# Optimization experiments

Hardware: AMD Instinct MI355X
Metric: run time of the kernel (lower is better)

## Reference

```python
import jax, jax.numpy as jnp
import numpy as np

N_NODES = 100_000
N_EDGES = 1_600_000
F_NODE = 4
F_EDGE = 5
H = 64
EDGE_DIM = 2 * H + F_EDGE  # 133


def setup_inputs() -> dict:
    key = jax.random.key(0)
    ks = jax.random.split(key, 24)
    s = 0.05
    inp = {
        "node_feat": jax.random.normal(ks[0], (N_NODES, F_NODE), jnp.float32),
        "edge_feat": jax.random.normal(ks[1], (N_EDGES, F_EDGE), jnp.float32),
        "src": jax.random.randint(ks[2], (N_EDGES,), 0, N_NODES, jnp.int32),
        "dst": jax.random.randint(ks[3], (N_EDGES,), 0, N_NODES, jnp.int32),
        # SAGEConv 1 (DGL mean aggregator: fc_self(h) + fc_neigh(mean_neigh(h)) + bias)
        "W1s": jax.random.normal(ks[4], (F_NODE, H), jnp.float32) * s,
        "W1n": jax.random.normal(ks[5], (F_NODE, H), jnp.float32) * s,
        "b1": jnp.zeros((H,), jnp.float32),
        # SAGEConv 2
        "W2s": jax.random.normal(ks[6], (H, H), jnp.float32) * s,
        "W2n": jax.random.normal(ks[7], (H, H), jnp.float32) * s,
        "b2": jnp.zeros((H,), jnp.float32),
        # nodeprocess: Linear(F_NODE? no -> applied to h which is H-dim) Linear(H? )
        # NOTE: original declares nn.Linear(num_node_features, hidden) but applies it to h (H-dim);
        # we follow the applied shape, Linear(H, H), so the math is runnable and consistent.
        "Wnp": jax.random.normal(ks[8], (H, H), jnp.float32) * s,
        "bnp": jnp.zeros((H,), jnp.float32),
        # edgeprocess: Linear(EDGE_DIM, H) -> tanh -> Linear(H, 1)
        "We1": jax.random.normal(ks[9], (EDGE_DIM, H), jnp.float32) * s,
        "be1": jnp.zeros((H,), jnp.float32),
        "We2": jax.random.normal(ks[10], (H, 1), jnp.float32) * s,
        "be2": jnp.zeros((1,), jnp.float32),
        # lin1: Linear(EDGE_DIM, H); lin2: Linear(H, 1)
        "Wl1": jax.random.normal(ks[11], (EDGE_DIM, H), jnp.float32) * s,
        "bl1": jnp.zeros((H,), jnp.float32),
        "Wl2": jax.random.normal(ks[12], (H, 1), jnp.float32) * s,
        "bl2": jnp.zeros((1,), jnp.float32),
    }
    return inp


def _sage_mean(h, src, dst, Ws, Wn, b, inv_deg):
    # project first (cheaper: N x d instead of E x d), then gather+scatter-mean
    msg = (h @ Wn)[src]                                    # [E, H]
    agg = jax.ops.segment_sum(msg, dst, num_segments=h.shape[0]) * inv_deg
    return h @ Ws + agg + b


def reference(node_feat, edge_feat, src, dst,
              W1s, W1n, b1, W2s, W2n, b2,
              Wnp, bnp, We1, be1, We2, be2,
              Wl1, bl1, Wl2, bl2):
    n = node_feat.shape[0]
    deg = jax.ops.segment_sum(jnp.ones_like(dst, jnp.float32), dst, num_segments=n)
    inv_deg = (1.0 / jnp.maximum(deg, 1.0))[:, None]       # [N,1]

    h = jax.nn.relu(_sage_mean(node_feat, src, dst, W1s, W1n, b1, inv_deg))
    h = jax.nn.relu(_sage_mean(h, src, dst, W2s, W2n, b2, inv_deg))

    h_src = jax.nn.relu(h[src] @ Wnp + bnp)                # [E, H]
    h_dst = jax.nn.relu(h[dst] @ Wnp + bnp)                # [E, H]
    ef = jnp.concatenate([h_src, h_dst, edge_feat], axis=1)  # [E, 133]

    w = jax.nn.sigmoid(jnp.tanh(ef @ We1 + be1) @ We2 + be2)  # [E, 1]
    efw = ef * w
    out = jax.nn.relu(efw @ Wl1 + bl1)                     # dropout: eval mode (identity)
    return out @ Wl2 + bl2                                 # [E, 1]
```

## Files before the change

### kernel.cpp

```cpp
#include <hip/hip_runtime.h>
#include <math.h>


__device__ __forceinline__ float fast_tanh(float x) {
    x = fminf(fmaxf(x, -15.f), 15.f);
    float e2 = __expf(2.f * x);
    return (e2 - 1.f) * __builtin_amdgcn_rcpf(e2 + 1.f);
}
__device__ __forceinline__ float fast_sigmoid(float x) {
    x = fminf(fmaxf(x, -60.f), 60.f);
    return __builtin_amdgcn_rcpf(1.f + __expf(-x));
}
__device__ __forceinline__ unsigned short f2bf(float f) {
    unsigned u = __float_as_uint(f);
    u = u + 0x7FFFu + ((u >> 16) & 1u);
    return (unsigned short)(u >> 16);
}
__device__ __forceinline__ unsigned pack2bf(float lo, float hi) {
    return ((unsigned)f2bf(hi) << 16) | (unsigned)f2bf(lo);
}
__device__ __forceinline__ float bflo(unsigned u) { return __uint_as_float(u << 16); }
__device__ __forceinline__ float bfhi(unsigned u) { return __uint_as_float(u & 0xFFFF0000u); }

__device__ __forceinline__ float dpp_sum16(float x) {
    int t;
    t = __builtin_amdgcn_update_dpp(0, __float_as_int(x), 0xB1, 0xF, 0xF, true);
    x += __int_as_float(t);
    t = __builtin_amdgcn_update_dpp(0, __float_as_int(x), 0x4E, 0xF, 0xF, true);
    x += __int_as_float(t);
    t = __builtin_amdgcn_update_dpp(0, __float_as_int(x), 0x141, 0xF, 0xF, true);
    x += __int_as_float(t);
    t = __builtin_amdgcn_update_dpp(0, __float_as_int(x), 0x140, 0xF, 0xF, true);
    x += __int_as_float(t);
    return x;
}

__global__ void rank_k(const int* __restrict__ dst, int* __restrict__ deg,
                       int* __restrict__ rank, int E) {
    int e = blockIdx.x * blockDim.x + threadIdx.x;
    if (e < E) rank[e] = atomicAdd(&deg[dst[e]], 1);
}

__global__ void scan1_k(const int* __restrict__ deg, int* __restrict__ off,
                        int* __restrict__ bsum, int N) {
    __shared__ int tmp[256];
    int i = blockIdx.x * 256 + threadIdx.x;
    int v = (i < N) ? deg[i] : 0;
    tmp[threadIdx.x] = v;
    __syncthreads();
#pragma unroll
    for (int s = 1; s < 256; s <<= 1) {
        int t = (threadIdx.x >= s) ? tmp[threadIdx.x - s] : 0;
        __syncthreads();
        tmp[threadIdx.x] += t;
        __syncthreads();
    }
    if (i < N) off[i] = tmp[threadIdx.x] - v;
    if (threadIdx.x == 255) bsum[blockIdx.x] = tmp[255];
}

__global__ void scan2_k(int* __restrict__ bsum, int nb) {
    __shared__ int tmp[512];
    int i = threadIdx.x;
    int v = (i < nb) ? bsum[i] : 0;
    tmp[i] = v;
    __syncthreads();
#pragma unroll
    for (int s = 1; s < 512; s <<= 1) {
        int t = (i >= s) ? tmp[i - s] : 0;
        __syncthreads();
        tmp[i] += t;
        __syncthreads();
    }
    if (i < nb) bsum[i] = tmp[i] - v;
}

__global__ void scan3_k(int* __restrict__ off, const int* __restrict__ bsum,
                        int N, int E) {
    int i = blockIdx.x * 256 + threadIdx.x;
    if (i < N) off[i] += bsum[blockIdx.x];
    if (i == 0) off[N] = E;
}

__global__ void fill2_k(const int* __restrict__ src, const int* __restrict__ dst,
                        const int* __restrict__ off, const int* __restrict__ rank,
                        int2* __restrict__ csr, int* __restrict__ dstp, int E) {
    int e = blockIdx.x * blockDim.x + threadIdx.x;
    if (e >= E) return;
    int d = dst[e];
    int pos = off[d] + rank[e];
    csr[pos] = make_int2(src[e], e);
    dstp[pos] = d;
}

__global__ __launch_bounds__(256, 8)
void aggh1f_k(const int* __restrict__ off, const int2* __restrict__ csr,
              const float* __restrict__ nf,
              const float* __restrict__ W1s, const float* __restrict__ W1n,
              const float* __restrict__ b1, unsigned* __restrict__ h1b, int N) {
    int n = blockIdx.x * 16 + (threadIdx.x >> 4);
    if (n >= N) return;
    int q = threadIdx.x & 15;
    int s0 = off[n], s1 = off[n + 1];
    const float4* nf4 = (const float4*)nf;
    float4 a = {0.f, 0.f, 0.f, 0.f};
    for (int i = s0 + q; i < s1; i += 16) {
        float4 r = nf4[(unsigned)csr[i].x];
        a.x += r.x; a.y += r.y; a.z += r.z; a.w += r.w;
    }
    a.x = dpp_sum16(a.x);
    a.y = dpp_sum16(a.y);
    a.z = dpp_sum16(a.z);
    a.w = dpp_sum16(a.w);
    float invd = 1.f / fmaxf((float)(s1 - s0), 1.f);
    a.x *= invd; a.y *= invd; a.z *= invd; a.w *= invd;
    float4 r = nf4[(unsigned)n];
    const int j0 = q << 2;
    float4 acc = *(const float4*)&b1[j0];
#pragma unroll
    for (int k = 0; k < 4; ++k) {
        float rk = (k == 0) ? r.x : (k == 1) ? r.y : (k == 2) ? r.z : r.w;
        float ak = (k == 0) ? a.x : (k == 1) ? a.y : (k == 2) ? a.z : a.w;
        float4 ws = *(const float4*)&W1s[k * 64 + j0];
        float4 wn = *(const float4*)&W1n[k * 64 + j0];
        acc.x = fmaf(rk, ws.x, acc.x); acc.y = fmaf(rk, ws.y, acc.y);
        acc.z = fmaf(rk, ws.z, acc.z); acc.w = fmaf(rk, ws.w, acc.w);
        acc.x = fmaf(ak, wn.x, acc.x); acc.y = fmaf(ak, wn.y, acc.y);
        acc.z = fmaf(ak, wn.z, acc.z); acc.w = fmaf(ak, wn.w, acc.w);
    }
    uint2 pk;
    pk.x = pack2bf(fmaxf(acc.x, 0.f), fmaxf(acc.y, 0.f));
    pk.y = pack2bf(fmaxf(acc.z, 0.f), fmaxf(acc.w, 0.f));
    *(uint2*)&h1b[(unsigned)n * 32u + (q << 1)] = pk;
}

__global__ __launch_bounds__(256, 8)
void gatherh1_k(const int* __restrict__ off, const int2* __restrict__ csr,
                const uint4* __restrict__ h1b4, uint4* __restrict__ ah1b4, int N) {
    int n = blockIdx.x * 4 + (threadIdx.x >> 6);
    if (n >= N) return;
    int l = threadIdx.x & 63;
    int g = l >> 3, q = l & 7;
    int s0 = off[n], s1 = off[n + 1];
    float a0 = 0.f, a1 = 0.f, a2 = 0.f, a3 = 0.f;
    float a4 = 0.f, a5 = 0.f, a6 = 0.f, a7 = 0.f;
    int i = s0;
    for (; i + 16 <= s1; i += 16) {
        int r0 = csr[i + g].x;
        int r1 = csr[i + 8 + g].x;
        uint4 v0 = h1b4[(unsigned)r0 * 8u + q];
        uint4 v1 = h1b4[(unsigned)r1 * 8u + q];
        a0 += bflo(v0.x) + bflo(v1.x); a1 += bfhi(v0.x) + bfhi(v1.x);
        a2 += bflo(v0.y) + bflo(v1.y); a3 += bfhi(v0.y) + bfhi(v1.y);
        a4 += bflo(v0.z) + bflo(v1.z); a5 += bfhi(v0.z) + bfhi(v1.z);
        a6 += bflo(v0.w) + bflo(v1.w); a7 += bfhi(v0.w) + bfhi(v1.w);
    }
    for (; i + 8 <= s1; i += 8) {
        int r = csr[i + g].x;
        uint4 v = h1b4[(unsigned)r * 8u + q];
        a0 += bflo(v.x); a1 += bfhi(v.x);
        a2 += bflo(v.y); a3 += bfhi(v.y);
        a4 += bflo(v.z); a5 += bfhi(v.z);
        a6 += bflo(v.w); a7 += bfhi(v.w);
    }
    int rem = s1 - i;
    if (g < rem) {
        int r = csr[i + g].x;
        uint4 v = h1b4[(unsigned)r * 8u + q];
        a0 += bflo(v.x); a1 += bfhi(v.x);
        a2 += bflo(v.y); a3 += bfhi(v.y);
        a4 += bflo(v.z); a5 += bfhi(v.z);
        a6 += bflo(v.w); a7 += bfhi(v.w);
    }
#pragma unroll
    for (int m = 8; m <= 32; m <<= 1) {
        a0 += __shfl_xor(a0, m); a1 += __shfl_xor(a1, m);
        a2 += __shfl_xor(a2, m); a3 += __shfl_xor(a3, m);
        a4 += __shfl_xor(a4, m); a5 += __shfl_xor(a5, m);
        a6 += __shfl_xor(a6, m); a7 += __shfl_xor(a7, m);
    }
    if (l < 8) {
        float invd = 1.f / fmaxf((float)(s1 - s0), 1.f);
        uint4 pk;
        pk.x = pack2bf(a0 * invd, a1 * invd);
        pk.y = pack2bf(a2 * invd, a3 * invd);
        pk.z = pack2bf(a4 * invd, a5 * invd);
        pk.w = pack2bf(a6 * invd, a7 * invd);
        ah1b4[(unsigned)n * 8u + q] = pk;
    }
}

__device__ __forceinline__ void mac64(const float (*hT)[68], const float (*wt)[64],
                                      int rr, int cr, float acc[4][4]) {
#pragma unroll 8
    for (int k = 0; k < 64; ++k) {
        float4 a = *(const float4*)&hT[k][rr];
        float4 w = *(const float4*)&wt[k][cr];
        acc[0][0] = fmaf(a.x, w.x, acc[0][0]); acc[0][1] = fmaf(a.x, w.y, acc[0][1]);
        acc[0][2] = fmaf(a.x, w.z, acc[0][2]); acc[0][3] = fmaf(a.x, w.w, acc[0][3]);
        acc[1][0] = fmaf(a.y, w.x, acc[1][0]); acc[1][1] = fmaf(a.y, w.y, acc[1][1]);
        acc[1][2] = fmaf(a.y, w.z, acc[1][2]); acc[1][3] = fmaf(a.y, w.w, acc[1][3]);
        acc[2][0] = fmaf(a.z, w.x, acc[2][0]); acc[2][1] = fmaf(a.z, w.y, acc[2][1]);
        acc[2][2] = fmaf(a.z, w.z, acc[2][2]); acc[2][3] = fmaf(a.z, w.w, acc[2][3]);
        acc[3][0] = fmaf(a.w, w.x, acc[3][0]); acc[3][1] = fmaf(a.w, w.y, acc[3][1]);
        acc[3][2] = fmaf(a.w, w.z, acc[3][2]); acc[3][3] = fmaf(a.w, w.w, acc[3][3]);
    }
}

__global__ __launch_bounds__(256, 4)
void node_mlp_k(const unsigned* __restrict__ h1b, const unsigned* __restrict__ ah1b,
                const float* __restrict__ W2s, const float* __restrict__ W2n,
                const float* __restrict__ b2, const float* __restrict__ Wnp,
                const float* __restrict__ bnp, const float* __restrict__ We1,
                const float* __restrict__ Wl1, const float* __restrict__ be1,
                unsigned short* __restrict__ ST, int N) {
    __shared__ __align__(16) float hT[64][68];
    __shared__ __align__(16) float wt[64][64];
    const int t = threadIdx.x;
    const int m0 = blockIdx.x * 64;
    const int cr = (t & 15) << 2, rr = (t >> 4) << 2;
    float acc[4][4] = {};

#pragma unroll
    for (int it = 0; it < 8; ++it) {
        int u = it * 256 + t;
        int m = u >> 5, p = u & 31;
        int row = m0 + m;
        unsigned v = (row < N) ? h1b[(unsigned)row * 32u + p] : 0u;
        hT[2 * p][m] = bflo(v);
        hT[2 * p + 1][m] = bfhi(v);
    }
#pragma unroll
    for (int it = 0; it < 16; ++it) {
        int k = it * 4 + (t >> 6), c = t & 63;
        wt[k][c] = W2s[k * 64 + c];
    }
    __syncthreads();
    mac64(hT, wt, rr, cr, acc);
    __syncthreads();

#pragma unroll
    for (int it = 0; it < 8; ++it) {
        int u = it * 256 + t;
        int m = u >> 5, p = u & 31;
        int row = m0 + m;
        unsigned v = (row < N) ? ah1b[(unsigned)row * 32u + p] : 0u;
        hT[2 * p][m] = bflo(v);
        hT[2 * p + 1][m] = bfhi(v);
    }
#pragma unroll
    for (int it = 0; it < 16; ++it) {
        int k = it * 4 + (t >> 6), c = t & 63;
        wt[k][c] = W2n[k * 64 + c];
    }
    __syncthreads();
    mac64(hT, wt, rr, cr, acc);
    __syncthreads();

#pragma unroll
    for (int i = 0; i < 4; ++i)
#pragma unroll
        for (int q = 0; q < 4; ++q)
            hT[cr + q][rr + i] = fmaxf(acc[i][q] + b2[cr + q], 0.f);
#pragma unroll
    for (int it = 0; it < 16; ++it) {
        int k = it * 4 + (t >> 6), c = t & 63;
        wt[k][c] = Wnp[k * 64 + c];
    }
    __syncthreads();
    float ac2[4][4] = {};
    mac64(hT, wt, rr, cr, ac2);
    __syncthreads();

#pragma unroll
    for (int i = 0; i < 4; ++i)
#pragma unroll
        for (int q = 0; q < 4; ++q)
            hT[cr + q][rr + i] = fmaxf(ac2[i][q] + bnp[cr + q], 0.f);
    __syncthreads();

    for (int cb = 0; cb < 4; ++cb) {
        if (cb) __syncthreads();
#pragma unroll
        for (int it = 0; it < 16; ++it) {
            int k = it * 4 + (t >> 6), c = t & 63;
            int cglob = cb * 64 + c;
            int half = cglob >> 7, cc = cglob & 127;
            int jj = cc >> 1, p = cc & 1;
            const float* W = p ? Wl1 : We1;
            wt[k][c] = W[(half * 64 + k) * 64 + jj];
        }
        __syncthreads();
        float ac3[4][4] = {};
        mac64(hT, wt, rr, cr, ac3);
        float bz0 = 0.f, bz2 = 0.f;
        if (cb >= 2) {
            int jj0 = ((cb * 64 + cr) & 127) >> 1;
            bz0 = be1[jj0];
            bz2 = be1[jj0 + 1];
        }
#pragma unroll
        for (int i = 0; i < 4; ++i) {
            int row = m0 + rr + i;
            if (row >= N) continue;
            ushort4 pk;
            pk.x = f2bf(ac3[i][0] + bz0); pk.y = f2bf(ac3[i][1]);
            pk.z = f2bf(ac3[i][2] + bz2); pk.w = f2bf(ac3[i][3]);
            *(ushort4*)&ST[(unsigned)row * 256u + cb * 64 + cr] = pk;
        }
    }
}

struct P8 {
    int2 seA, seB;
    int dnA, dnB;
    uint4 pwA, swA, pwB, swB;
    float eA0, eA1, eA2, eA3, eA4;
    float eB0, eB1, eB2, eB3, eB4;
    bool actA, actB;
};

__device__ __forceinline__ P8 pref_pair(int c, int nwaves, int nch, int E,
                                        int g, int j0,
                                        const int2* __restrict__ csr,
                                        const int* __restrict__ dstp,
                                        const float* __restrict__ ef,
                                        const unsigned* __restrict__ ST32) {
    P8 p;
    int sA = c * 4 + g;
    int cB = c + nwaves;
    int sB = cB * 4 + g;
    p.actA = (c < nch) && (sA < E);
    p.actB = (cB < nch) && (sB < E);
    unsigned uA = p.actA ? (unsigned)sA : 0u;
    unsigned uB = p.actB ? (unsigned)sB : 0u;
    p.dnA = dstp[uA];
    p.dnB = dstp[uB];
    p.seA = csr[uA];
    p.seB = csr[uB];
    p.pwA = *(const uint4*)&ST32[(unsigned)p.dnA * 128u + 64u + (unsigned)j0];
    p.pwB = *(const uint4*)&ST32[(unsigned)p.dnB * 128u + 64u + (unsigned)j0];
    p.swA = *(const uint4*)&ST32[(unsigned)p.seA.x * 128u + (unsigned)j0];
    p.swB = *(const uint4*)&ST32[(unsigned)p.seB.x * 128u + (unsigned)j0];
    const float* epA = ef + (unsigned)p.seA.y * 5u;
    const float* epB = ef + (unsigned)p.seB.y * 5u;
    p.eA0 = epA[0]; p.eA1 = epA[1]; p.eA2 = epA[2]; p.eA3 = epA[3]; p.eA4 = epA[4];
    p.eB0 = epB[0]; p.eB1 = epB[1]; p.eB2 = epB[2]; p.eB3 = epB[3]; p.eB4 = epB[4];
    return p;
}

__global__ void edge_k(const int2* __restrict__ csr, const int* __restrict__ dstp,
                       const float* __restrict__ ef, const unsigned* __restrict__ ST32,
                       const float* __restrict__ We1,
                       const float* __restrict__ We2, const float* __restrict__ be2,
                       const float* __restrict__ Wl1, const float* __restrict__ bl1,
                       const float* __restrict__ Wl2, const float* __restrict__ bl2,
                       float* __restrict__ out, int E, int nwaves) {
    const int l = threadIdx.x & 63;
    const int g = l >> 4;
    const int q = l & 15;
    const int j0 = q << 2;
    const int wid = blockIdx.x * (blockDim.x >> 6) + (threadIdx.x >> 6);

    float4 wet[5], wlt[5];
#pragma unroll
    for (int k = 0; k < 5; ++k) {
        wet[k] = *(const float4*)&We1[(128 + k) * 64 + j0];
        wlt[k] = *(const float4*)&Wl1[(128 + k) * 64 + j0];
    }
    const float4 vwe2 = *(const float4*)&We2[j0];
    const float4 vbl1 = *(const float4*)&bl1[j0];
    const float4 vwl2 = *(const float4*)&Wl2[j0];
    const float vbe2 = be2[0], vbl2 = bl2[0];

    const int nch = (E + 3) >> 2;
    const int step = 2 * nwaves;

#define KS(EK, K) \
    t4.x = fmaf(EK, wet[K].x, t4.x); t4.y = fmaf(EK, wet[K].y, t4.y); \
    t4.z = fmaf(EK, wet[K].z, t4.z); t4.w = fmaf(EK, wet[K].w, t4.w); \
    u4.x = fmaf(EK, wlt[K].x, u4.x); u4.y = fmaf(EK, wlt[K].y, u4.y); \
    u4.z = fmaf(EK, wlt[K].z, u4.z); u4.w = fmaf(EK, wlt[K].w, u4.w);

    P8 p = pref_pair(wid, nwaves, nch, E, g, j0, csr, dstp, ef, ST32);
    for (int c = wid; c < nch; ) {
        int cn = c + step;
        P8 pn = pref_pair(cn, nwaves, nch, E, g, j0, csr, dstp, ef, ST32);

        {
            float4 t4 = {bflo(p.swA.x) + bflo(p.pwA.x),
                         bflo(p.swA.y) + bflo(p.pwA.y),
                         bflo(p.swA.z) + bflo(p.pwA.z),
                         bflo(p.swA.w) + bflo(p.pwA.w)};
            float4 u4 = {bfhi(p.swA.x) + bfhi(p.pwA.x), bfhi(p.swA.y) + bfhi(p.pwA.y),
                         bfhi(p.swA.z) + bfhi(p.pwA.z), bfhi(p.swA.w) + bfhi(p.pwA.w)};
            KS(p.eA0, 0) KS(p.eA1, 1) KS(p.eA2, 2) KS(p.eA3, 3) KS(p.eA4, 4)
            float z = fast_tanh(t4.x) * vwe2.x + fast_tanh(t4.y) * vwe2.y
                    + fast_tanh(t4.z) * vwe2.z + fast_tanh(t4.w) * vwe2.w;
            z = dpp_sum16(z);
            float w = fast_sigmoid(z + vbe2);
            float o = fmaxf(fmaf(w, u4.x, vbl1.x), 0.f) * vwl2.x
                    + fmaxf(fmaf(w, u4.y, vbl1.y), 0.f) * vwl2.y
                    + fmaxf(fmaf(w, u4.z, vbl1.z), 0.f) * vwl2.z
                    + fmaxf(fmaf(w, u4.w, vbl1.w), 0.f) * vwl2.w;
            o = dpp_sum16(o);
            if (q == 0 && p.actA) out[(unsigned)p.seA.y] = o + vbl2;
        }
        {
            float4 t4 = {bflo(p.swB.x) + bflo(p.pwB.x),
                         bflo(p.swB.y) + bflo(p.pwB.y),
                         bflo(p.swB.z) + bflo(p.pwB.z),
                         bflo(p.swB.w) + bflo(p.pwB.w)};
            float4 u4 = {bfhi(p.swB.x) + bfhi(p.pwB.x), bfhi(p.swB.y) + bfhi(p.pwB.y),
                         bfhi(p.swB.z) + bfhi(p.pwB.z), bfhi(p.swB.w) + bfhi(p.pwB.w)};
            KS(p.eB0, 0) KS(p.eB1, 1) KS(p.eB2, 2) KS(p.eB3, 3) KS(p.eB4, 4)
            float z = fast_tanh(t4.x) * vwe2.x + fast_tanh(t4.y) * vwe2.y
                    + fast_tanh(t4.z) * vwe2.z + fast_tanh(t4.w) * vwe2.w;
            z = dpp_sum16(z);
            float w = fast_sigmoid(z + vbe2);
            float o = fmaxf(fmaf(w, u4.x, vbl1.x), 0.f) * vwl2.x
                    + fmaxf(fmaf(w, u4.y, vbl1.y), 0.f) * vwl2.y
                    + fmaxf(fmaf(w, u4.z, vbl1.z), 0.f) * vwl2.z
                    + fmaxf(fmaf(w, u4.w, vbl1.w), 0.f) * vwl2.w;
            o = dpp_sum16(o);
            if (q == 0 && p.actB) out[(unsigned)p.seB.y] = o + vbl2;
        }
        p = pn;
        c = cn;
    }
#undef KS
}

extern "C" void kernel_launch(void* const* d_in, const int* in_sizes, int n_in,
                              void* d_out, int out_size, void* d_ws, size_t ws_size,
                              hipStream_t stream) {
    const float* nf  = (const float*)d_in[0];
    const float* ef  = (const float*)d_in[1];
    const int*   src = (const int*)d_in[2];
    const int*   dst = (const int*)d_in[3];
    const float* W1s = (const float*)d_in[4];
    const float* W1n = (const float*)d_in[5];
    const float* b1  = (const float*)d_in[6];
    const float* W2s = (const float*)d_in[7];
    const float* W2n = (const float*)d_in[8];
    const float* b2  = (const float*)d_in[9];
    const float* Wnp = (const float*)d_in[10];
    const float* bnp = (const float*)d_in[11];
    const float* We1 = (const float*)d_in[12];
    const float* be1 = (const float*)d_in[13];
    const float* We2 = (const float*)d_in[14];
    const float* be2 = (const float*)d_in[15];
    const float* Wl1 = (const float*)d_in[16];
    const float* bl1 = (const float*)d_in[17];
    const float* Wl2 = (const float*)d_in[18];
    const float* bl2 = (const float*)d_in[19];

    const int N = in_sizes[0] / 4;
    const int E = in_sizes[2];

    float* wsf = (float*)d_ws;
    unsigned short* ST = (unsigned short*)wsf;
    unsigned* ah1b = (unsigned*)(wsf + (size_t)128 * N);
    int* dstp = (int*)(wsf + (size_t)160 * N);
    unsigned* h1b  = (unsigned*)(wsf + (size_t)192 * N);
    int2* csr  = (int2*)(wsf + (size_t)224 * N);
    int*  rank = (int*)(wsf + (size_t)256 * N);
    int*  deg  = (int*)(wsf + (size_t)272 * N);
    int*  off  = deg + N;
    int*  bsum = off + N + 1;
    float* out = (float*)d_out;

    const int nblkN1 = (N + 255) / 256;
    const int nblkE  = (E + 255) / 256;
    const int nblkNw4 = (N + 3) / 4;
    const int nblkN16 = (N + 15) / 16;
    const int gemmx  = (N + 63) / 64;
    const int EDGE_BLOCKS = 3072;
    const int nwaves = EDGE_BLOCKS * 4;

    hipMemsetAsync(deg, 0, (size_t)N * sizeof(int), stream);
    rank_k<<<nblkE, 256, 0, stream>>>(dst, deg, rank, E);
    scan1_k<<<nblkN1, 256, 0, stream>>>(deg, off, bsum, N);
    scan2_k<<<1, 512, 0, stream>>>(bsum, nblkN1);
    scan3_k<<<nblkN1, 256, 0, stream>>>(off, bsum, N, E);
    fill2_k<<<nblkE, 256, 0, stream>>>(src, dst, off, rank, csr, dstp, E);

    aggh1f_k<<<nblkN16, 256, 0, stream>>>(off, csr, nf, W1s, W1n, b1, h1b, N);

    gatherh1_k<<<nblkNw4, 256, 0, stream>>>(off, csr, (const uint4*)h1b,
                                            (uint4*)ah1b, N);

    node_mlp_k<<<gemmx, 256, 0, stream>>>(h1b, ah1b, W2s, W2n, b2,
                                          Wnp, bnp, We1, Wl1, be1, ST, N);

    edge_k<<<EDGE_BLOCKS, 256, 0, stream>>>(csr, dstp, ef, (const unsigned*)ST,
                                            We1, We2, be2, Wl1, bl1, Wl2, bl2,
                                            out, E, nwaves);
}
```

Baseline: 502.3 us.

## Port node MLP to bf16 MFMA with split hi/lo weight precision

Replaces the fp32 FMA-based node MLP GEMMs with 16x16x32 bf16 MFMA instructions. Weights are pre-split into bf16 hi and lo parts in a MFMA-fragment layout by a new small prep kernel, and intermediate activations are split into hi and lo in LDS, so accuracy approaches fp32 with about three MFMAs per product. The goal is to cut the ALU and LDS cost of the node-level dense layers. It adds a kernel launch and a weight-prep pass on every call, and reads the weight fragments directly from global memory.

```diff
diff --git a/kernel.cpp b/kernel.cpp
--- a/kernel.cpp
+++ b/kernel.cpp
@@ -1,6 +1,9 @@
 #include <hip/hip_runtime.h>
 #include <math.h>
 
+
+typedef __attribute__((ext_vector_type(8))) short bf16x8;
+typedef __attribute__((ext_vector_type(4))) float f32x4;
 
 __device__ __forceinline__ float fast_tanh(float x) {
     x = fminf(fmaxf(x, -15.f), 15.f);
@@ -21,6 +24,14 @@
 }
 __device__ __forceinline__ float bflo(unsigned u) { return __uint_as_float(u << 16); }
 __device__ __forceinline__ float bfhi(unsigned u) { return __uint_as_float(u & 0xFFFF0000u); }
+__device__ __forceinline__ float bf2f(unsigned short h) {
+    return __uint_as_float((unsigned)h << 16);
+}
+
+__device__ __forceinline__ f32x4 mfma16(uint4 a, uint4 b, f32x4 c) {
+    return __builtin_amdgcn_mfma_f32_16x16x32_bf16(
+        __builtin_bit_cast(bf16x8, a), __builtin_bit_cast(bf16x8, b), c, 0, 0, 0);
+}
 
 __device__ __forceinline__ float dpp_sum16(float x) {
     int t;
@@ -91,6 +102,53 @@
     int pos = off[d] + rank[e];
     csr[pos] = make_int2(src[e], e);
     dstp[pos] = d;
+}
+
+__global__ void prep_w_k(const float* __restrict__ W2s, const float* __restrict__ W2n,
+                         const float* __restrict__ Wnp, const float* __restrict__ We1,
+                         const float* __restrict__ Wl1, uint4* __restrict__ w2sF,
+                         uint4* __restrict__ w2nF, uint4* __restrict__ wnpF,
+                         uint4* __restrict__ wbigF) {
+    const int b = blockIdx.x, t = threadIdx.x;
+    if (b < 3) {
+        const float* W = (b == 0) ? W2s : (b == 1) ? W2n : Wnp;
+        uint4* out = (b == 0) ? w2sF : (b == 1) ? w2nF : wnpF;
+        for (int u = t; u < 2 * 4 * 64; u += 256) {
+            int l = u & 63, nt = (u >> 6) & 3, ks = u >> 8;
+            int m = nt * 16 + (l & 15), kb = ks * 32 + (l >> 4) * 8;
+            unsigned hi[4], lo[4];
+#pragma unroll
+            for (int jp = 0; jp < 4; ++jp) {
+                float v0 = W[(kb + 2 * jp) * 64 + m];
+                float v1 = W[(kb + 2 * jp + 1) * 64 + m];
+                unsigned short h0 = f2bf(v0), h1 = f2bf(v1);
+                unsigned short q0 = f2bf(v0 - bf2f(h0)), q1 = f2bf(v1 - bf2f(h1));
+                hi[jp] = ((unsigned)h1 << 16) | h0;
+                lo[jp] = ((unsigned)q1 << 16) | q0;
+            }
+            out[u * 2]     = make_uint4(hi[0], hi[1], hi[2], hi[3]);
+            out[u * 2 + 1] = make_uint4(lo[0], lo[1], lo[2], lo[3]);
+        }
+    } else {
+        for (int u = t; u < 2 * 16 * 64; u += 256) {
+            int l = u & 63, nt = (u >> 6) & 15, ks = u >> 10;
+            int m = nt * 16 + (l & 15), kb = ks * 32 + (l >> 4) * 8;
+            int half = m >> 7, cc = m & 127, jj = cc >> 1, p = cc & 1;
+            const float* W = p ? Wl1 : We1;
+            unsigned hi[4], lo[4];
+#pragma unroll
+            for (int jp = 0; jp < 4; ++jp) {
+                float v0 = W[(half * 64 + kb + 2 * jp) * 64 + jj];
+                float v1 = W[(half * 64 + kb + 2 * jp + 1) * 64 + jj];
+                unsigned short h0 = f2bf(v0), h1 = f2bf(v1);
+                unsigned short q0 = f2bf(v0 - bf2f(h0)), q1 = f2bf(v1 - bf2f(h1));
+                hi[jp] = ((unsigned)h1 << 16) | h0;
+                lo[jp] = ((unsigned)q1 << 16) | q0;
+            }
+            wbigF[u * 2]     = make_uint4(hi[0], hi[1], hi[2], hi[3]);
+            wbigF[u * 2 + 1] = make_uint4(lo[0], lo[1], lo[2], lo[3]);
+        }
+    }
 }
 
 __global__ __launch_bounds__(256, 8)
@@ -190,123 +248,136 @@
     }
 }
 
-__device__ __forceinline__ void mac64(const float (*hT)[68], const float (*wt)[64],
-                                      int rr, int cr, float acc[4][4]) {
-#pragma unroll 8
-    for (int k = 0; k < 64; ++k) {
-        float4 a = *(const float4*)&hT[k][rr];
-        float4 w = *(const float4*)&wt[k][cr];
-        acc[0][0] = fmaf(a.x, w.x, acc[0][0]); acc[0][1] = fmaf(a.x, w.y, acc[0][1]);
-        acc[0][2] = fmaf(a.x, w.z, acc[0][2]); acc[0][3] = fmaf(a.x, w.w, acc[0][3]);
-        acc[1][0] = fmaf(a.y, w.x, acc[1][0]); acc[1][1] = fmaf(a.y, w.y, acc[1][1]);
-        acc[1][2] = fmaf(a.y, w.z, acc[1][2]); acc[1][3] = fmaf(a.y, w.w, acc[1][3]);
-        acc[2][0] = fmaf(a.z, w.x, acc[2][0]); acc[2][1] = fmaf(a.z, w.y, acc[2][1]);
-        acc[2][2] = fmaf(a.z, w.z, acc[2][2]); acc[2][3] = fmaf(a.z, w.w, acc[2][3]);
-        acc[3][0] = fmaf(a.w, w.x, acc[3][0]); acc[3][1] = fmaf(a.w, w.y, acc[3][1]);
-        acc[3][2] = fmaf(a.w, w.z, acc[3][2]); acc[3][3] = fmaf(a.w, w.w, acc[3][3]);
-    }
-}
-
-__global__ __launch_bounds__(256, 4)
-void node_mlp_k(const unsigned* __restrict__ h1b, const unsigned* __restrict__ ah1b,
-                const float* __restrict__ W2s, const float* __restrict__ W2n,
-                const float* __restrict__ b2, const float* __restrict__ Wnp,
-                const float* __restrict__ bnp, const float* __restrict__ We1,
-                const float* __restrict__ Wl1, const float* __restrict__ be1,
-                unsigned short* __restrict__ ST, int N) {
-    __shared__ __align__(16) float hT[64][68];
-    __shared__ __align__(16) float wt[64][64];
+__global__ __launch_bounds__(256)
+void node_mlp_mfma_k(const uint4* __restrict__ h1v, const uint4* __restrict__ ahv,
+                     const uint4* __restrict__ w2sF, const uint4* __restrict__ w2nF,
+                     const uint4* __restrict__ wnpF, const uint4* __restrict__ wbigF,
+                     const float* __restrict__ b2, const float* __restrict__ bnp,
+                     const float* __restrict__ be1, unsigned short* __restrict__ ST,
+                     int N) {
+    __shared__ __align__(16) unsigned short Ahi[64][72];
+    __shared__ __align__(16) unsigned short Alo[64][72];
     const int t = threadIdx.x;
+    const int w = t >> 6, l = t & 63;
+    const int lr = l & 15, kq = l >> 4;
     const int m0 = blockIdx.x * 64;
-    const int cr = (t & 15) << 2, rr = (t >> 4) << 2;
-    float acc[4][4] = {};
-
-#pragma unroll
-    for (int it = 0; it < 8; ++it) {
-        int u = it * 256 + t;
-        int m = u >> 5, p = u & 31;
-        int row = m0 + m;
-        unsigned v = (row < N) ? h1b[(unsigned)row * 32u + p] : 0u;
-        hT[2 * p][m] = bflo(v);
-        hT[2 * p + 1][m] = bfhi(v);
-    }
-#pragma unroll
-    for (int it = 0; it < 16; ++it) {
-        int k = it * 4 + (t >> 6), c = t & 63;
-        wt[k][c] = W2s[k * 64 + c];
+    const int gr = m0 + w * 16 + lr;
+    const bool inb = gr < N;
+    const int prow = w * 16 + lr;
+    const int cbq = kq * 4;
+
+    const uint4 z4 = make_uint4(0u, 0u, 0u, 0u);
+
+    uint4 x1[2], xa[2];
+#pragma unroll
+    for (int ks = 0; ks < 2; ++ks) {
+        unsigned idx = (unsigned)gr * 8u + (unsigned)(ks * 4 + kq);
+        x1[ks] = inb ? h1v[idx] : z4;
+        xa[ks] = inb ? ahv[idx] : z4;
+    }
+
+    f32x4 acc[4];
+#pragma unroll
+    for (int nt = 0; nt < 4; ++nt) acc[nt] = (f32x4){0.f, 0.f, 0.f, 0.f};
+#pragma unroll
+    for (int ks = 0; ks < 2; ++ks)
+#pragma unroll
+        for (int nt = 0; nt < 4; ++nt) {
+            int base = ((ks * 4 + nt) * 64 + l) * 2;
+            acc[nt] = mfma16(w2sF[base],     x1[ks], acc[nt]);
+            acc[nt] = mfma16(w2sF[base + 1], x1[ks], acc[nt]);
+            acc[nt] = mfma16(w2nF[base],     xa[ks], acc[nt]);
+            acc[nt] = mfma16(w2nF[base + 1], xa[ks], acc[nt]);
+        }
+#pragma unroll
+    for (int nt = 0; nt < 4; ++nt) {
+        float4 vb = *(const float4*)&b2[nt * 16 + cbq];
+        float v0 = fmaxf(acc[nt][0] + vb.x, 0.f);
+        float v1 = fmaxf(acc[nt][1] + vb.y, 0.f);
+        float v2 = fmaxf(acc[nt][2] + vb.z, 0.f);
+        float v3 = fmaxf(acc[nt][3] + vb.w, 0.f);
+        unsigned short h0 = f2bf(v0), h1 = f2bf(v1), h2 = f2bf(v2), h3 = f2bf(v3);
+        unsigned short q0 = f2bf(v0 - bf2f(h0)), q1 = f2bf(v1 - bf2f(h1));
+        unsigned short q2 = f2bf(v2 - bf2f(h2)), q3 = f2bf(v3 - bf2f(h3));
+        *(uint2*)&Ahi[prow][nt * 16 + cbq] =
+            make_uint2(((unsigned)h1 << 16) | h0, ((unsigned)h3 << 16) | h2);
+        *(uint2*)&Alo[prow][nt * 16 + cbq] =
+            make_uint2(((unsigned)q1 << 16) | q0, ((unsigned)q3 << 16) | q2);
     }
     __syncthreads();
-    mac64(hT, wt, rr, cr, acc);
+
+    uint4 ahi2[2], alo2[2];
+#pragma unroll
+    for (int ks = 0; ks < 2; ++ks) {
+        ahi2[ks] = *(const uint4*)&Ahi[prow][ks * 32 + kq * 8];
+        alo2[ks] = *(const uint4*)&Alo[prow][ks * 32 + kq * 8];
+    }
+
+    f32x4 a3[4];
+#pragma unroll
+    for (int nt = 0; nt < 4; ++nt) a3[nt] = (f32x4){0.f, 0.f, 0.f, 0.f};
+#pragma unroll
+    for (int ks = 0; ks < 2; ++ks)
+#pragma unroll
+        for (int nt = 0; nt < 4; ++nt) {
+            int base = ((ks * 4 + nt) * 64 + l) * 2;
+            a3[nt] = mfma16(wnpF[base],     ahi2[ks], a3[nt]);
+            a3[nt] = mfma16(wnpF[base + 1], ahi2[ks], a3[nt]);
+            a3[nt] = mfma16(wnpF[base],     alo2[ks], a3[nt]);
+        }
+#pragma unroll
+    for (int nt = 0; nt < 4; ++nt) {
+        float4 vb = *(const float4*)&bnp[nt * 16 + cbq];
+        float v0 = fmaxf(a3[nt][0] + vb.x, 0.f);
+        float v1 = fmaxf(a3[nt][1] + vb.y, 0.f);
+        float v2 = fmaxf(a3[nt][2] + vb.z, 0.f);
+        float v3 = fmaxf(a3[nt][3] + vb.w, 0.f);
+        unsigned short h0 = f2bf(v0), h1 = f2bf(v1), h2 = f2bf(v2), h3 = f2bf(v3);
+        unsigned short q0 = f2bf(v0 - bf2f(h0)), q1 = f2bf(v1 - bf2f(h1));
+        unsigned short q2 = f2bf(v2 - bf2f(h2)), q3 = f2bf(v3 - bf2f(h3));
+        *(uint2*)&Ahi[prow][nt * 16 + cbq] =
+            make_uint2(((unsigned)h1 << 16) | h0, ((unsigned)h3 << 16) | h2);
+        *(uint2*)&Alo[prow][nt * 16 + cbq] =
+            make_uint2(((unsigned)q1 << 16) | q0, ((unsigned)q3 << 16) | q2);
+    }
     __syncthreads();
 
-#pragma unroll
-    for (int it = 0; it < 8; ++it) {
-        int u = it * 256 + t;
-        int m = u >> 5, p = u & 31;
-        int row = m0 + m;
-        unsigned v = (row < N) ? ah1b[(unsigned)row * 32u + p] : 0u;
-        hT[2 * p][m] = bflo(v);
-        hT[2 * p + 1][m] = bfhi(v);
-    }
-#pragma unroll
-    for (int it = 0; it < 16; ++it) {
-        int k = it * 4 + (t >> 6), c = t & 63;
-        wt[k][c] = W2n[k * 64 + c];
-    }
-    __syncthreads();
-    mac64(hT, wt, rr, cr, acc);
-    __syncthreads();
-
-#pragma unroll
-    for (int i = 0; i < 4; ++i)
-#pragma unroll
-        for (int q = 0; q < 4; ++q)
-            hT[cr + q][rr + i] = fmaxf(acc[i][q] + b2[cr + q], 0.f);
-#pragma unroll
-    for (int it = 0; it < 16; ++it) {
-        int k = it * 4 + (t >> 6), c = t & 63;
-        wt[k][c] = Wnp[k * 64 + c];
-    }
-    __syncthreads();
-    float ac2[4][4] = {};
-    mac64(hT, wt, rr, cr, ac2);
-    __syncthreads();
-
-#pragma unroll
-    for (int i = 0; i < 4; ++i)
-#pragma unroll
-        for (int q = 0; q < 4; ++q)
-            hT[cr + q][rr + i] = fmaxf(ac2[i][q] + bnp[cr + q], 0.f);
-    __syncthreads();
-
-    for (int cb = 0; cb < 4; ++cb) {
-        if (cb) __syncthreads();
-#pragma unroll
-        for (int it = 0; it < 16; ++it) {
-            int k = it * 4 + (t >> 6), c = t & 63;
-            int cglob = cb * 64 + c;
-            int half = cglob >> 7, cc = cglob & 127;
-            int jj = cc >> 1, p = cc & 1;
-            const float* W = p ? Wl1 : We1;
-            wt[k][c] = W[(half * 64 + k) * 64 + jj];
-        }
-        __syncthreads();
-        float ac3[4][4] = {};
-        mac64(hT, wt, rr, cr, ac3);
-        float bz0 = 0.f, bz2 = 0.f;
-        if (cb >= 2) {
-            int jj0 = ((cb * 64 + cr) & 127) >> 1;
-            bz0 = be1[jj0];
-            bz2 = be1[jj0 + 1];
-        }
-#pragma unroll
-        for (int i = 0; i < 4; ++i) {
-            int row = m0 + rr + i;
-            if (row >= N) continue;
+    uint4 bhi[2], blo[2];
+#pragma unroll
+    for (int ks = 0; ks < 2; ++ks) {
+        bhi[ks] = *(const uint4*)&Ahi[prow][ks * 32 + kq * 8];
+        blo[ks] = *(const uint4*)&Alo[prow][ks * 32 + kq * 8];
+    }
+
+#pragma unroll
+    for (int mtg = 0; mtg < 4; ++mtg) {
+        f32x4 a4[4];
+#pragma unroll
+        for (int m4 = 0; m4 < 4; ++m4) a4[m4] = (f32x4){0.f, 0.f, 0.f, 0.f};
+#pragma unroll
+        for (int m4 = 0; m4 < 4; ++m4) {
+            int mt = mtg * 4 + m4;
+#pragma unroll
+            for (int ks = 0; ks < 2; ++ks) {
+                int base = ((ks * 16 + mt) * 64 + l) * 2;
+                a4[m4] = mfma16(wbigF[base],     bhi[ks], a4[m4]);
+                a4[m4] = mfma16(wbigF[base + 1], bhi[ks], a4[m4]);
+                a4[m4] = mfma16(wbigF[base],     blo[ks], a4[m4]);
+            }
+        }
+#pragma unroll
+        for (int m4 = 0; m4 < 4; ++m4) {
+            int mt = mtg * 4 + m4;
+            int stcb = mt * 16 + cbq;
+            float v0 = a4[m4][0], v1 = a4[m4][1], v2 = a4[m4][2], v3 = a4[m4][3];
+            if (mt >= 8) {
+                int jj0 = (mt - 8) * 8 + kq * 2;
+                v0 += be1[jj0];
+                v2 += be1[jj0 + 1];
+            }
             ushort4 pk;
-            pk.x = f2bf(ac3[i][0] + bz0); pk.y = f2bf(ac3[i][1]);
-            pk.z = f2bf(ac3[i][2] + bz2); pk.w = f2bf(ac3[i][3]);
-            *(ushort4*)&ST[(unsigned)row * 256u + cb * 64 + cr] = pk;
+            pk.x = f2bf(v0); pk.y = f2bf(v1); pk.z = f2bf(v2); pk.w = f2bf(v3);
+            if (inb) *(ushort4*)&ST[(unsigned)gr * 256u + (unsigned)stcb] = pk;
         }
     }
 }
@@ -462,6 +533,10 @@
     unsigned short* ST = (unsigned short*)wsf;
     unsigned* ah1b = (unsigned*)(wsf + (size_t)128 * N);
     int* dstp = (int*)(wsf + (size_t)160 * N);
+    uint4* w2sF  = (uint4*)(wsf + (size_t)176 * N);
+    uint4* w2nF  = w2sF + 1024;
+    uint4* wnpF  = w2sF + 2048;
+    uint4* wbigF = w2sF + 3072;
     unsigned* h1b  = (unsigned*)(wsf + (size_t)192 * N);
     int2* csr  = (int2*)(wsf + (size_t)224 * N);
     int*  rank = (int*)(wsf + (size_t)256 * N);
@@ -478,6 +553,9 @@
     const int EDGE_BLOCKS = 3072;
     const int nwaves = EDGE_BLOCKS * 4;
 
+    prep_w_k<<<4, 256, 0, stream>>>(W2s, W2n, Wnp, We1, Wl1,
+                                    w2sF, w2nF, wnpF, wbigF);
+
     hipMemsetAsync(deg, 0, (size_t)N * sizeof(int), stream);
     rank_k<<<nblkE, 256, 0, stream>>>(dst, deg, rank, E);
     scan1_k<<<nblkN1, 256, 0, stream>>>(deg, off, bsum, N);
@@ -490,8 +568,9 @@
     gatherh1_k<<<nblkNw4, 256, 0, stream>>>(off, csr, (const uint4*)h1b,
                                             (uint4*)ah1b, N);
 
-    node_mlp_k<<<gemmx, 256, 0, stream>>>(h1b, ah1b, W2s, W2n, b2,
-                                          Wnp, bnp, We1, Wl1, be1, ST, N);
+    node_mlp_mfma_k<<<gemmx, 256, 0, stream>>>((const uint4*)h1b, (const uint4*)ah1b,
+                                               w2sF, w2nF, wnpF, wbigF,
+                                               b2, bnp, be1, ST, N);
 
     edge_k<<<EDGE_BLOCKS, 256, 0, stream>>>(csr, dstp, ef, (const unsigned*)ST,
                                             We1, We2, be2, Wl1, bl1, Wl2, bl2,
```

Measured after the change: 476.0 us. 5.2% less time.
